# Optimization experiments

Hardware: AMD Instinct MI355X
Metric: run time of the kernel (lower is better)

The kernel has to match this reference:

```python
import jax, jax.numpy as jnp
import numpy as np

N_QUBITS = 14      # must be even (module assert)
IN_CHANNEL = 512   # batch of independent circuits

# PennyLane convention: wire 0 is the most-significant bit of the basis index.

def _mcx_perm(n, c1, c2, t):
    # MultiControlledX with control_values '10': flip target bit t when bit(c1)==1 and bit(c2)==0
    idx = np.arange(2 ** n)
    b1 = (idx >> (n - 1 - c1)) & 1
    b2 = (idx >> (n - 1 - c2)) & 1
    return np.where((b1 == 1) & (b2 == 0), idx ^ (1 << (n - 1 - t)), idx)

_MCX_PERMS = [jnp.asarray(_mcx_perm(N_QUBITS, w, (w + 1) % N_QUBITS, (w + 2) % N_QUBITS))
              for w in range(N_QUBITS)]
# Z-eigenvalue signs per basis state per wire: (2^n, n)
_Z_SIGNS = jnp.asarray(
    np.stack([1.0 - 2.0 * ((np.arange(2 ** N_QUBITS) >> (N_QUBITS - 1 - w)) & 1)
              for w in range(N_QUBITS)], axis=1), dtype=jnp.float32)


def _apply_rx(state, theta, w):
    # RX(theta) = [[cos(t/2), -i sin(t/2)], [-i sin(t/2), cos(t/2)]] on wire w; theta: (B,)
    B = state.shape[0]
    st = state.reshape(B, 2 ** w, 2, -1)
    c = jnp.cos(0.5 * theta)[:, None, None]
    s = (-1j * jnp.sin(0.5 * theta))[:, None, None]
    s0, s1 = st[:, :, 0, :], st[:, :, 1, :]
    out = jnp.stack([c * s0 + s * s1, c * s1 + s * s0], axis=2)
    return out.reshape(B, -1)


def _apply_rz(state, theta, w):
    # RZ(theta) = diag(e^{-i t/2}, e^{+i t/2}) on wire w
    B = state.shape[0]
    st = state.reshape(B, 2 ** w, 2, -1)
    p0 = jnp.exp(-0.5j * theta)[:, None, None]
    p1 = jnp.exp(0.5j * theta)[:, None, None]
    out = jnp.stack([p0 * st[:, :, 0, :], p1 * st[:, :, 1, :]], axis=2)
    return out.reshape(B, -1)


def _apply_isingxx(state, phi, wa, wb):
    a, b = min(wa, wb), max(wa, wb)
    B = state.shape[0]
    st = state.reshape(B, 2 ** a, 2, 2 ** (b - a - 1), 2, -1)
    c = jnp.cos(0.5 * phi)[:, None, None, None]
    s = (-1j * jnp.sin(0.5 * phi))[:, None, None, None]
    s00 = st[:, :, 0, :, 0, :]; s01 = st[:, :, 0, :, 1, :]
    s10 = st[:, :, 1, :, 0, :]; s11 = st[:, :, 1, :, 1, :]
    row0 = jnp.stack([c * s00 + s * s11, c * s01 + s * s10], axis=3)  # (B, 2^a, M, 2, R)
    row1 = jnp.stack([c * s10 + s * s01, c * s11 + s * s00], axis=3)
    return jnp.stack([row0, row1], axis=2).reshape(B, -1)


def _circuit(cp, p):
    n = N_QUBITS
    B = cp.shape[0]
    state = jnp.zeros((B, 2 ** n), dtype=jnp.complex64).at[:, 0].set(1.0)
    for w in range(n):
        state = _apply_rx(state, p[:, 0, w], w)
    for ws in range(n // 2):
        state = _apply_isingxx(state, cp[:, ws], 2 * ws, 2 * ws + 1)
    for w in range(n):
        state = _apply_rz(state, p[:, 1, w], w)
    for ws in range(n // 2):
        wss = 2 * ws + 1
        state = _apply_isingxx(state, cp[:, ws + n // 2], wss, (wss + 1) % n)
    for w in range(n):
        state = _apply_rx(state, p[:, 2, w], w)
    for w in range(n):
        state = state[:, _MCX_PERMS[w]]
    probs = state.real ** 2 + state.imag ** 2  # (B, 2^n)
    return (probs @ _Z_SIGNS).astype(jnp.float32)  # (B, n) = expval PauliZ per wire


def setup_inputs() -> dict:
    key = jax.random.key(0)
    k1, k2 = jax.random.split(key)
    cp = jax.random.uniform(k1, (IN_CHANNEL, N_QUBITS), dtype=jnp.float32) * jnp.pi
    p = jax.random.uniform(k2, (IN_CHANNEL, 3, N_QUBITS), dtype=jnp.float32) * jnp.pi
    return {"cp": cp, "p": p}


def reference(cp, p):
    return _circuit(cp, p)
```

## Files before the change

### kernel.cpp

```cpp
#include <hip/hip_runtime.h>

#define NQ 14
#define NSTATE (1 << NQ)
#define NT 256
#define AMPS 64

typedef float  f2  __attribute__((ext_vector_type(2)));
typedef __fp16 h2v __attribute__((ext_vector_type(2)));

#define N_H2 16640
#define OFF_BTAB  (N_H2*4)
#define OFF_RX3   (OFF_BTAB + 28*8)
#define OFF_XX2   (OFF_RX3 + 28*4)
#define OFF_RED   (OFF_XX2 + 14*4)
#define SMEM_BYTES (OFF_RED + 4*NQ*4)

__device__ __forceinline__ f2 cmul(f2 a, f2 b){
    f2 br = {-b.y, b.x};
    return a.x * b + a.y * br;
}

__device__ __forceinline__ f2 pkswz(f2 ss, f2 y){
    f2 t;
    asm("v_pk_mul_f32 %0, %1, %2 op_sel:[0,1] op_sel_hi:[1,0] neg_hi:[0,1]"
        : "=v"(t) : "v"(ss), "v"(y));
    return t;
}
__device__ __forceinline__ f2 pkfma(f2 a, f2 b, f2 c){
    f2 d;
    asm("v_pk_fma_f32 %0, %1, %2, %3" : "=v"(d) : "v"(a), "v"(b), "v"(c));
    return d;
}
__device__ __forceinline__ void rot2(f2& A, f2& B, f2 cc, f2 ss){
    f2 tA = pkswz(ss, B);
    f2 tB = pkswz(ss, A);
    A = pkfma(cc, A, tA);
    B = pkfma(cc, B, tB);
}

__device__ __forceinline__ h2v pack(f2 v){ return __builtin_amdgcn_cvt_pkrtz(v.x, v.y); }
__device__ __forceinline__ f2  unpack(h2v h){ return (f2){(float)h.x, (float)h.y}; }

template<int CTRL>
__device__ __forceinline__ f2 qperm(f2 v){
    int x = __builtin_amdgcn_mov_dpp(__float_as_int(v.x), CTRL, 0xf, 0xf, true);
    int y = __builtin_amdgcn_mov_dpp(__float_as_int(v.y), CTRL, 0xf, 0xf, true);
    return (f2){__int_as_float(x), __int_as_float(y)};
}

template<int P, int M>
__device__ __forceinline__ void applyXX(f2* amp, f2 cc, f2 ss){
    #pragma unroll
    for (int L = 0; L < AMPS; ++L)
        if (!((L >> P) & 1)) rot2(amp[L], amp[L ^ M], cc, ss);
}
template<int R>
__device__ __forceinline__ void applyRX(f2* amp, f2 cc, f2 ss){
    #pragma unroll
    for (int L = 0; L < AMPS; ++L)
        if (!((L >> R) & 1)) rot2(amp[L], amp[L | (1 << R)], cc, ss);
}

__global__ void perm_tbl_kernel(unsigned short* __restrict__ tbl)
{
    const int j = blockIdx.x * blockDim.x + threadIdx.x;
    int x = j;
    #pragma unroll
    for (int w = 0; w < NQ; ++w) {
        const int p1 = 13 - w;
        const int p2 = 13 - ((w + 1) % NQ);
        const int pt = 13 - ((w + 2) % NQ);
        const int cond = ((x >> p1) & ~(x >> p2)) & 1;
        x ^= cond << pt;
    }
    const int L  = (j >> 1) & 63;
    const int l  = (j & 1) | (((j >> 13) & 1) << 1) | (((j >> 12) & 1) << 2)
                 | (((j >> 11) & 1) << 3) | (((j >> 10) & 1) << 4) | (((j >> 9) & 1) << 5);
    const int w_ = (((j >> 7) & 1) << 1) | ((j >> 8) & 1);
    const int t  = (w_ << 6) | l;
    tbl[(L >> 3) * 2048 + t * 8 + (L & 7)] = (unsigned short)x;
}

__global__ void __launch_bounds__(NT, 2)
qsim_kernel(const float* __restrict__ cp, const float* __restrict__ p,
            const unsigned short* __restrict__ tblD, float* __restrict__ out)
{
    extern __shared__ __align__(16) char smem[];
    h2v* st    = reinterpret_cast<h2v*>(smem);
    f2*  Btab  = reinterpret_cast<f2*>(smem + OFF_BTAB);
    float* rx3c = reinterpret_cast<float*>(smem + OFF_RX3);
    float* rx3s = rx3c + 14;
    float* xx2c = reinterpret_cast<float*>(smem + OFF_XX2);
    float* xx2s = xx2c + 7;
    float* red  = reinterpret_cast<float*>(smem + OFF_RED);

    const int b = blockIdx.x;
    const int t = threadIdx.x;
    const float* pb  = p  + b * 42;
    const float* cpb = cp + b * 14;

    if (t < 7) {
        const int ws = t, wa = 2*ws, wb = 2*ws + 1;
        float sa, ca; sincosf(0.5f * pb[wa], &sa, &ca);
        float sb, cb; sincosf(0.5f * pb[wb], &sb, &cb);
        f2 s00 = {ca*cb, 0.f};
        f2 s01 = {0.f, -ca*sb};
        f2 s10 = {0.f, -sa*cb};
        f2 s11 = {-sa*sb, 0.f};
        float sx, cx; sincosf(0.5f * cpb[ws], &sx, &cx);
        rot2(s00, s11, (f2){cx,cx}, (f2){sx,sx});
        rot2(s01, s10, (f2){cx,cx}, (f2){sx,sx});
        const float ga = 0.5f * pb[14 + wa], gb = 0.5f * pb[14 + wb];
        float sA, cA; sincosf(ga + gb, &sA, &cA);
        float sB, cB; sincosf(gb - ga, &sB, &cB);
        s00 = cmul(s00, (f2){cA, -sA});
        s11 = cmul(s11, (f2){cA,  sA});
        s01 = cmul(s01, (f2){cB,  sB});
        s10 = cmul(s10, (f2){cB, -sB});
        const int k = 6 - ws;
        Btab[k*4+0] = s00; Btab[k*4+1] = s01; Btab[k*4+2] = s10; Btab[k*4+3] = s11;
    } else if (t >= 64 && t < 78) {
        const int w = t - 64;
        float s, c; sincosf(0.5f * pb[28 + w], &s, &c);
        rx3c[w] = c; rx3s[w] = s;
    } else if (t >= 128 && t < 135) {
        const int g = t - 128;
        float s, c; sincosf(0.5f * cpb[7 + g], &s, &c);
        xx2c[g] = c; xx2s[g] = s;
    }
    __syncthreads();

    f2 amp[AMPS];
    f2 cc, ss;
    #define LOADXX(g) do { float c_ = xx2c[g], s_ = xx2s[g]; cc = (f2){c_,c_}; ss = (f2){s_,s_}; } while (0)
    #define LOADRX(w) do { float c_ = rx3c[w], s_ = rx3s[w]; cc = (f2){c_,c_}; ss = (f2){s_,s_}; } while (0)

    {
        const int t6 = (t >> 6) & 1, t7 = t >> 7;
        f2 Pc = cmul(cmul(Btab[t & 3], Btab[4 + ((t >> 2) & 3)]), Btab[8 + ((t >> 4) & 3)]);
        f2 P3a0 = cmul(Pc, Btab[12 + t6]);
        f2 P3a1 = cmul(Pc, Btab[12 + 2 + t6]);
        f2 G00 = cmul(P3a0, Btab[24 + (t7 << 1)]);
        f2 G01 = cmul(P3a0, Btab[24 + (t7 << 1) + 1]);
        f2 G10 = cmul(P3a1, Btab[24 + (t7 << 1)]);
        f2 G11 = cmul(P3a1, Btab[24 + (t7 << 1) + 1]);
        #pragma unroll
        for (int m = 0; m < 16; ++m) {
            f2 H = cmul(Btab[16 + (m & 3)], Btab[20 + (m >> 2)]);
            amp[(m << 1)]          = cmul(G00, H);
            amp[(m << 1) | 1]      = cmul(G10, H);
            amp[32 | (m << 1)]     = cmul(G01, H);
            amp[32 | (m << 1) | 1] = cmul(G11, H);
        }
        LOADXX(0); applyXX<5, 0x30>(amp, cc, ss);
        LOADXX(1); applyXX<3, 0x0C>(amp, cc, ss);
        LOADXX(2); applyXX<1, 0x03>(amp, cc, ss);
        LOADRX(1); applyRX<5>(amp, cc, ss);
        LOADRX(2); applyRX<4>(amp, cc, ss);
        LOADRX(3); applyRX<3>(amp, cc, ss);
        LOADRX(4); applyRX<2>(amp, cc, ss);
        LOADRX(5); applyRX<1>(amp, cc, ss);
        LOADRX(6); applyRX<0>(amp, cc, ss);
        const int jhi = (t7 << 13) | (t & 127);
        #pragma unroll
        for (int L = 0; L < AMPS; ++L) {
            const int j = jhi | (L << 7);
            st[j ^ ((j >> 9) & 31)] = pack(amp[L]);
        }
    }
    __syncthreads();

    {
        uint4 tv[8];
        const uint4* tq = reinterpret_cast<const uint4*>(tblD);
        #pragma unroll
        for (int g = 0; g < 8; ++g) tv[g] = tq[g * 256 + t];

        const int l = t & 63, w_ = t >> 6;
        const int jbase = (l & 1) | (((w_ >> 1) & 1) << 7) | ((w_ & 1) << 8)
                        | (((l >> 5) & 1) << 9) | (((l >> 4) & 1) << 10)
                        | (((l >> 3) & 1) << 11) | (((l >> 2) & 1) << 12)
                        | (((l >> 1) & 1) << 13);
        const int jb2 = jbase ^ ((jbase >> 9) & 31);
        #pragma unroll
        for (int L = 0; L < AMPS; ++L)
            amp[L] = unpack(st[jb2 ^ (L << 1)]);
        LOADXX(3); applyXX<5, 0x30>(amp, cc, ss);
        LOADXX(4); applyXX<3, 0x0C>(amp, cc, ss);
        LOADXX(5); applyXX<1, 0x03>(amp, cc, ss);
        LOADRX(7);  applyRX<5>(amp, cc, ss);
        LOADRX(8);  applyRX<4>(amp, cc, ss);
        LOADRX(9);  applyRX<3>(amp, cc, ss);
        LOADRX(10); applyRX<2>(amp, cc, ss);
        LOADRX(11); applyRX<1>(amp, cc, ss);
        LOADRX(12); applyRX<0>(amp, cc, ss);
        LOADXX(6);
        #pragma unroll
        for (int L = 0; L < AMPS; ++L) { f2 pv = qperm<0x1B>(amp[L]); amp[L] = pkfma(cc, amp[L], pkswz(ss, pv)); }
        LOADRX(13);
        #pragma unroll
        for (int L = 0; L < AMPS; ++L) { f2 pv = qperm<0xB1>(amp[L]); amp[L] = pkfma(cc, amp[L], pkswz(ss, pv)); }
        LOADRX(0);
        #pragma unroll
        for (int L = 0; L < AMPS; ++L) { f2 pv = qperm<0x4E>(amp[L]); amp[L] = pkfma(cc, amp[L], pkswz(ss, pv)); }
        __syncthreads();
        #pragma unroll
        for (int L = 0; L < AMPS; ++L) {
            const unsigned comp = (L & 4) ? ((L & 2) ? tv[L >> 3].w : tv[L >> 3].z)
                                          : ((L & 2) ? tv[L >> 3].y : tv[L >> 3].x);
            const unsigned f = (L & 1) ? (comp >> 16) : (comp & 0xffffu);
            st[f + (f >> 6)] = pack(amp[L]);
        }
    }
    __syncthreads();

    {
        const h2v* erow = st + t * 65;
        float U0, U1 = 0.f, U2 = 0.f, U4, U5, T;
        float C[8];
        float u0acc = 0.f;
        #pragma unroll
        for (int ch = 0; ch < 8; ++ch) {
            float q[8];
            #pragma unroll
            for (int e = 0; e < 8; ++e) {
                const f2 a = unpack(erow[ch * 8 + e]);
                q[e] = fmaf(a.x, a.x, a.y * a.y);
            }
            const float p0 = q[0] + q[1], p1 = q[2] + q[3], p2 = q[4] + q[5], p3 = q[6] + q[7];
            u0acc += (q[1] + q[3]) + (q[5] + q[7]);
            U1 += p1 + p3;
            const float s01 = p0 + p1, s23 = p2 + p3;
            U2 += s23;
            C[ch] = s01 + s23;
        }
        U0 = u0acc;
        {
            const float P0 = C[0] + C[1], P1 = C[2] + C[3], P2 = C[4] + C[5], P3v = C[6] + C[7];
            const float U3v = (C[1] + C[3]) + (C[5] + C[7]);
            U4 = P1 + P3v;
            const float Q0 = P0 + P1, Q1 = P2 + P3v;
            U5 = Q1;
            T = Q0 + Q1;
            C[0] = U3v;
        }
        const float U3 = C[0];

        float s = T;
        float d0, d1, d2, d3, d4, d5;
        {
            float o;
            o = __shfl_xor(s, 1);  d0 = s - o; s += o;
            o = __shfl_xor(d0, 2); d0 += o;
            o = __shfl_xor(s, 2);  d1 = s - o; s += o;
            o = __shfl_xor(d0, 4); d0 += o;
            o = __shfl_xor(d1, 4); d1 += o;
            o = __shfl_xor(s, 4);  d2 = s - o; s += o;
            o = __shfl_xor(d0, 8); d0 += o;
            o = __shfl_xor(d1, 8); d1 += o;
            o = __shfl_xor(d2, 8); d2 += o;
            o = __shfl_xor(s, 8);  d3 = s - o; s += o;
            o = __shfl_xor(d0, 16); d0 += o;
            o = __shfl_xor(d1, 16); d1 += o;
            o = __shfl_xor(d2, 16); d2 += o;
            o = __shfl_xor(d3, 16); d3 += o;
            o = __shfl_xor(s, 16);  d4 = s - o; s += o;
            o = __shfl_xor(d0, 32); d0 += o;
            o = __shfl_xor(d1, 32); d1 += o;
            o = __shfl_xor(d2, 32); d2 += o;
            o = __shfl_xor(d3, 32); d3 += o;
            o = __shfl_xor(d4, 32); d4 += o;
            o = __shfl_xor(s, 32);  d5 = s - o; s += o;
        }
        float V0 = U0, V1 = U1, V2 = U2, V3 = U3, V4 = U4, V5 = U5;
        #pragma unroll
        for (int m = 1; m < 64; m <<= 1) {
            V0 += __shfl_xor(V0, m);
            V1 += __shfl_xor(V1, m);
            V2 += __shfl_xor(V2, m);
            V3 += __shfl_xor(V3, m);
            V4 += __shfl_xor(V4, m);
            V5 += __shfl_xor(V5, m);
        }
        if ((t & 63) == 0) {
            const int wv = t >> 6;
            float* r = red + wv * NQ;
            r[0]  = (wv & 2) ? -s : s;
            r[1]  = (wv & 1) ? -s : s;
            r[2]  = d5;
            r[3]  = d4;
            r[4]  = d3;
            r[5]  = d2;
            r[6]  = d1;
            r[7]  = d0;
            r[8]  = s - 2.f * V5;
            r[9]  = s - 2.f * V4;
            r[10] = s - 2.f * V3;
            r[11] = s - 2.f * V2;
            r[12] = s - 2.f * V1;
            r[13] = s - 2.f * V0;
        }
    }
    __syncthreads();
    if (t < NQ) {
        out[b * NQ + t] = (red[t] + red[NQ + t]) + (red[2 * NQ + t] + red[3 * NQ + t]);
    }
    #undef LOADXX
    #undef LOADRX
}

extern "C" void kernel_launch(void* const* d_in, const int* in_sizes, int n_in,
                              void* d_out, int out_size, void* d_ws, size_t ws_size,
                              hipStream_t stream)
{
    (void)n_in; (void)out_size; (void)ws_size;
    const float* cp = (const float*)d_in[0];
    const float* p  = (const float*)d_in[1];
    float* out = (float*)d_out;
    unsigned short* tbl = (unsigned short*)d_ws;
    const int B = in_sizes[0] / NQ;

    perm_tbl_kernel<<<NSTATE / 256, 256, 0, stream>>>(tbl);

    (void)hipFuncSetAttribute(reinterpret_cast<const void*>(qsim_kernel),
                              hipFuncAttributeMaxDynamicSharedMemorySize, SMEM_BYTES);
    qsim_kernel<<<B, NT, SMEM_BYTES, stream>>>(cp, p, tbl, out);
}
```

Baseline: 80.16 us.

## Rebalance gate split across phases and switch to vectorized swizzled LDS layout

Moves the second XX ring gate and two RX gates into the first register phase by using DPP quad permutes, which rebalances the work between the two LDS transposes. The first store now writes 16-byte packed vectors with an XOR swizzle. The permutation table is re-indexed so each thread loads its own contiguous entries, and the final reduction reads uint4 rows with a padding of 4 per 64 elements. Intra-quad reductions use DPP instead of ds_swizzle shuffles. Shared memory grows slightly, and the remapped index math carries a correctness risk.

Result: faster. 75.44 us (-5.9%).

```diff
diff --git a/kernel.cpp b/kernel.cpp
--- a/kernel.cpp
+++ b/kernel.cpp
@@ -8,7 +8,7 @@
 typedef float  f2  __attribute__((ext_vector_type(2)));
 typedef __fp16 h2v __attribute__((ext_vector_type(2)));
 
-#define N_H2 16640
+#define N_H2 17408
 #define OFF_BTAB  (N_H2*4)
 #define OFF_RX3   (OFF_BTAB + 28*8)
 #define OFF_XX2   (OFF_RX3 + 28*4)
@@ -19,7 +19,6 @@
     f2 br = {-b.y, b.x};
     return a.x * b + a.y * br;
 }
-
 __device__ __forceinline__ f2 pkswz(f2 ss, f2 y){
     f2 t;
     asm("v_pk_mul_f32 %0, %1, %2 op_sel:[0,1] op_sel_hi:[1,0] neg_hi:[0,1]"
@@ -37,15 +36,19 @@
     A = pkfma(cc, A, tA);
     B = pkfma(cc, B, tB);
 }
-
 __device__ __forceinline__ h2v pack(f2 v){ return __builtin_amdgcn_cvt_pkrtz(v.x, v.y); }
 __device__ __forceinline__ f2  unpack(h2v h){ return (f2){(float)h.x, (float)h.y}; }
+__device__ __forceinline__ f2  unpack_u(unsigned w){ h2v h = __builtin_bit_cast(h2v, w); return unpack(h); }
 
 template<int CTRL>
 __device__ __forceinline__ f2 qperm(f2 v){
     int x = __builtin_amdgcn_mov_dpp(__float_as_int(v.x), CTRL, 0xf, 0xf, true);
     int y = __builtin_amdgcn_mov_dpp(__float_as_int(v.y), CTRL, 0xf, 0xf, true);
     return (f2){__int_as_float(x), __int_as_float(y)};
+}
+template<int CTRL>
+__device__ __forceinline__ float fdpp(float v){
+    return __int_as_float(__builtin_amdgcn_mov_dpp(__float_as_int(v), CTRL, 0xf, 0xf, true));
 }
 
 template<int P, int M>
@@ -73,12 +76,9 @@
         const int cond = ((x >> p1) & ~(x >> p2)) & 1;
         x ^= cond << pt;
     }
-    const int L  = (j >> 1) & 63;
-    const int l  = (j & 1) | (((j >> 13) & 1) << 1) | (((j >> 12) & 1) << 2)
-                 | (((j >> 11) & 1) << 3) | (((j >> 10) & 1) << 4) | (((j >> 9) & 1) << 5);
-    const int w_ = (((j >> 7) & 1) << 1) | ((j >> 8) & 1);
-    const int t  = (w_ << 6) | l;
-    tbl[(L >> 3) * 2048 + t * 8 + (L & 7)] = (unsigned short)x;
+    const int t2 = (j >> 5) & 0xFF;
+    const int Lp = ((j >> 13) & 1) | ((j & 31) << 1);
+    tbl[t2 * 64 + Lp] = (unsigned short)x;
 }
 
 __global__ void __launch_bounds__(NT, 2)
@@ -86,8 +86,9 @@
             const unsigned short* __restrict__ tblD, float* __restrict__ out)
 {
     extern __shared__ __align__(16) char smem[];
-    h2v* st    = reinterpret_cast<h2v*>(smem);
-    f2*  Btab  = reinterpret_cast<f2*>(smem + OFF_BTAB);
+    h2v*   st   = reinterpret_cast<h2v*>(smem);
+    uint4* stq  = reinterpret_cast<uint4*>(smem);
+    f2*    Btab = reinterpret_cast<f2*>(smem + OFF_BTAB);
     float* rx3c = reinterpret_cast<float*>(smem + OFF_RX3);
     float* rx3s = rx3c + 14;
     float* xx2c = reinterpret_cast<float*>(smem + OFF_XX2);
@@ -117,8 +118,8 @@
         s11 = cmul(s11, (f2){cA,  sA});
         s01 = cmul(s01, (f2){cB,  sB});
         s10 = cmul(s10, (f2){cB, -sB});
-        const int k = 6 - ws;
-        Btab[k*4+0] = s00; Btab[k*4+1] = s01; Btab[k*4+2] = s10; Btab[k*4+3] = s11;
+        const int g = 6 - ws;
+        Btab[g*4+0] = s00; Btab[g*4+1] = s01; Btab[g*4+2] = s10; Btab[g*4+3] = s11;
     } else if (t >= 64 && t < 78) {
         const int w = t - 64;
         float s, c; sincosf(0.5f * pb[28 + w], &s, &c);
@@ -136,130 +137,128 @@
     #define LOADRX(w) do { float c_ = rx3c[w], s_ = rx3s[w]; cc = (f2){c_,c_}; ss = (f2){s_,s_}; } while (0)
 
     {
-        const int t6 = (t >> 6) & 1, t7 = t >> 7;
-        f2 Pc = cmul(cmul(Btab[t & 3], Btab[4 + ((t >> 2) & 3)]), Btab[8 + ((t >> 4) & 3)]);
-        f2 P3a0 = cmul(Pc, Btab[12 + t6]);
-        f2 P3a1 = cmul(Pc, Btab[12 + 2 + t6]);
-        f2 G00 = cmul(P3a0, Btab[24 + (t7 << 1)]);
-        f2 G01 = cmul(P3a0, Btab[24 + (t7 << 1) + 1]);
-        f2 G10 = cmul(P3a1, Btab[24 + (t7 << 1)]);
-        f2 G11 = cmul(P3a1, Btab[24 + (t7 << 1) + 1]);
+        const int i0 = (((t >> 5) & 1) << 1) | ((t >> 6) & 1);
+        const int i1 = (((t >> 3) & 1) << 1) | ((t >> 4) & 1);
+        const int i2 = (((t >> 1) & 1) << 1) | ((t >> 2) & 1);
+        f2 U = cmul(cmul(Btab[i0], Btab[4 + i1]), Btab[8 + i2]);
+        f2 B3v0 = Btab[12 + (t & 1)];
+        f2 B3v1 = Btab[12 + 2 + (t & 1)];
+        f2 B6v0 = Btab[24 + (((t >> 7) & 1) << 1)];
+        f2 B6v1 = Btab[24 + (((t >> 7) & 1) << 1) + 1];
+        f2 UB0 = cmul(U, B3v0), UB1 = cmul(U, B3v1);
+        f2 W00 = cmul(UB0, B6v0), W01 = cmul(UB1, B6v0);
+        f2 W10 = cmul(UB0, B6v1), W11 = cmul(UB1, B6v1);
         #pragma unroll
         for (int m = 0; m < 16; ++m) {
-            f2 H = cmul(Btab[16 + (m & 3)], Btab[20 + (m >> 2)]);
-            amp[(m << 1)]          = cmul(G00, H);
-            amp[(m << 1) | 1]      = cmul(G10, H);
-            amp[32 | (m << 1)]     = cmul(G01, H);
-            amp[32 | (m << 1) | 1] = cmul(G11, H);
+            f2 H = cmul(Btab[20 + (m >> 2)], Btab[16 + (m & 3)]);
+            amp[(m << 1)]          = cmul(W00, H);
+            amp[(m << 1) | 1]      = cmul(W01, H);
+            amp[32 | (m << 1)]     = cmul(W10, H);
+            amp[32 | (m << 1) | 1] = cmul(W11, H);
         }
         LOADXX(0); applyXX<5, 0x30>(amp, cc, ss);
         LOADXX(1); applyXX<3, 0x0C>(amp, cc, ss);
         LOADXX(2); applyXX<1, 0x03>(amp, cc, ss);
+        LOADXX(3);
+        #pragma unroll
+        for (int L = 0; L < AMPS; ++L) { f2 pv = qperm<0x1B>(amp[L]); amp[L] = pkfma(cc, amp[L], pkswz(ss, pv)); }
         LOADRX(1); applyRX<5>(amp, cc, ss);
         LOADRX(2); applyRX<4>(amp, cc, ss);
         LOADRX(3); applyRX<3>(amp, cc, ss);
         LOADRX(4); applyRX<2>(amp, cc, ss);
         LOADRX(5); applyRX<1>(amp, cc, ss);
         LOADRX(6); applyRX<0>(amp, cc, ss);
-        const int jhi = (t7 << 13) | (t & 127);
-        #pragma unroll
-        for (int L = 0; L < AMPS; ++L) {
-            const int j = jhi | (L << 7);
-            st[j ^ ((j >> 9) & 31)] = pack(amp[L]);
+        LOADRX(7);
+        #pragma unroll
+        for (int L = 0; L < AMPS; ++L) { f2 pv = qperm<0xB1>(amp[L]); amp[L] = pkfma(cc, amp[L], pkswz(ss, pv)); }
+        LOADRX(8);
+        #pragma unroll
+        for (int L = 0; L < AMPS; ++L) { f2 pv = qperm<0x4E>(amp[L]); amp[L] = pkfma(cc, amp[L], pkswz(ss, pv)); }
+        const int w1h = ((t & 1) | ((t >> 1) & 1) << 1 | (((t ^ (t >> 1) ^ (t >> 2)) & 1) << 2));
+        #pragma unroll
+        for (int m = 0; m < 16; ++m) {
+            uint4 pk;
+            pk.x = __builtin_bit_cast(unsigned, pack(amp[4*m]));
+            pk.y = __builtin_bit_cast(unsigned, pack(amp[4*m + 1]));
+            pk.z = __builtin_bit_cast(unsigned, pack(amp[4*m + 2]));
+            pk.w = __builtin_bit_cast(unsigned, pack(amp[4*m + 3]));
+            stq[t * 16 + (m ^ w1h)] = pk;
         }
     }
     __syncthreads();
 
     {
         uint4 tv[8];
-        const uint4* tq = reinterpret_cast<const uint4*>(tblD);
-        #pragma unroll
-        for (int g = 0; g < 8; ++g) tv[g] = tq[g * 256 + t];
-
-        const int l = t & 63, w_ = t >> 6;
-        const int jbase = (l & 1) | (((w_ >> 1) & 1) << 7) | ((w_ & 1) << 8)
-                        | (((l >> 5) & 1) << 9) | (((l >> 4) & 1) << 10)
-                        | (((l >> 3) & 1) << 11) | (((l >> 2) & 1) << 12)
-                        | (((l >> 1) & 1) << 13);
-        const int jb2 = jbase ^ ((jbase >> 9) & 31);
-        #pragma unroll
-        for (int L = 0; L < AMPS; ++L)
-            amp[L] = unpack(st[jb2 ^ (L << 1)]);
-        LOADXX(3); applyXX<5, 0x30>(amp, cc, ss);
-        LOADXX(4); applyXX<3, 0x0C>(amp, cc, ss);
-        LOADXX(5); applyXX<1, 0x03>(amp, cc, ss);
-        LOADRX(7);  applyRX<5>(amp, cc, ss);
-        LOADRX(8);  applyRX<4>(amp, cc, ss);
-        LOADRX(9);  applyRX<3>(amp, cc, ss);
-        LOADRX(10); applyRX<2>(amp, cc, ss);
-        LOADRX(11); applyRX<1>(amp, cc, ss);
-        LOADRX(12); applyRX<0>(amp, cc, ss);
-        LOADXX(6);
-        #pragma unroll
-        for (int L = 0; L < AMPS; ++L) { f2 pv = qperm<0x1B>(amp[L]); amp[L] = pkfma(cc, amp[L], pkswz(ss, pv)); }
-        LOADRX(13);
-        #pragma unroll
-        for (int L = 0; L < AMPS; ++L) { f2 pv = qperm<0xB1>(amp[L]); amp[L] = pkfma(cc, amp[L], pkswz(ss, pv)); }
-        LOADRX(0);
-        #pragma unroll
-        for (int L = 0; L < AMPS; ++L) { f2 pv = qperm<0x4E>(amp[L]); amp[L] = pkfma(cc, amp[L], pkswz(ss, pv)); }
+        {
+            const uint4* tq = reinterpret_cast<const uint4*>(tblD) + t * 8;
+            #pragma unroll
+            for (int g = 0; g < 8; ++g) tv[g] = tq[g];
+        }
+        const int sw2 = ((t & 2) >> 1) | ((t & 1) << 1);
+        const int Lf  = t >> 2;
+        const int w1b = ((sw2 & 1) << 2) | (((sw2 >> 1) & 1) << 3) | ((((sw2 ^ (sw2 >> 1)) & 1)) << 4);
+        #pragma unroll
+        for (int Lp = 0; Lp < AMPS; ++Lp) {
+            const int rev = ((Lp >> 5) & 1) | (((Lp >> 4) & 1) << 1) | (((Lp >> 3) & 1) << 2)
+                          | (((Lp >> 2) & 1) << 3) | (((Lp >> 1) & 1) << 4) | ((Lp & 1) << 5);
+            const int t1  = sw2 | (rev << 2);
+            const int w1v = w1b ^ ((rev & 1) << 4);
+            amp[Lp] = unpack(st[t1 * 64 + (Lf ^ w1v)]);
+        }
+        LOADXX(4); applyXX<5, 0x30>(amp, cc, ss);
+        LOADXX(5); applyXX<3, 0x0C>(amp, cc, ss);
+        LOADXX(6); applyXX<1, 0x03>(amp, cc, ss);
+        LOADRX(9);  applyRX<5>(amp, cc, ss);
+        LOADRX(10); applyRX<4>(amp, cc, ss);
+        LOADRX(11); applyRX<3>(amp, cc, ss);
+        LOADRX(12); applyRX<2>(amp, cc, ss);
+        LOADRX(13); applyRX<1>(amp, cc, ss);
+        LOADRX(0);  applyRX<0>(amp, cc, ss);
         __syncthreads();
         #pragma unroll
-        for (int L = 0; L < AMPS; ++L) {
-            const unsigned comp = (L & 4) ? ((L & 2) ? tv[L >> 3].w : tv[L >> 3].z)
-                                          : ((L & 2) ? tv[L >> 3].y : tv[L >> 3].x);
-            const unsigned f = (L & 1) ? (comp >> 16) : (comp & 0xffffu);
-            st[f + (f >> 6)] = pack(amp[L]);
+        for (int Lp = 0; Lp < AMPS; ++Lp) {
+            const unsigned word = (Lp & 4) ? ((Lp & 2) ? tv[Lp >> 3].w : tv[Lp >> 3].z)
+                                           : ((Lp & 2) ? tv[Lp >> 3].y : tv[Lp >> 3].x);
+            const unsigned f = (Lp & 1) ? (word >> 16) : (word & 0xffffu);
+            st[f + 4 * (f >> 6)] = pack(amp[Lp]);
         }
     }
     __syncthreads();
 
     {
-        const h2v* erow = st + t * 65;
-        float U0, U1 = 0.f, U2 = 0.f, U4, U5, T;
-        float C[8];
-        float u0acc = 0.f;
-        #pragma unroll
-        for (int ch = 0; ch < 8; ++ch) {
-            float q[8];
-            #pragma unroll
-            for (int e = 0; e < 8; ++e) {
-                const f2 a = unpack(erow[ch * 8 + e]);
-                q[e] = fmaf(a.x, a.x, a.y * a.y);
-            }
-            const float p0 = q[0] + q[1], p1 = q[2] + q[3], p2 = q[4] + q[5], p3 = q[6] + q[7];
-            u0acc += (q[1] + q[3]) + (q[5] + q[7]);
-            U1 += p1 + p3;
-            const float s01 = p0 + p1, s23 = p2 + p3;
-            U2 += s23;
-            C[ch] = s01 + s23;
-        }
-        U0 = u0acc;
-        {
-            const float P0 = C[0] + C[1], P1 = C[2] + C[3], P2 = C[4] + C[5], P3v = C[6] + C[7];
-            const float U3v = (C[1] + C[3]) + (C[5] + C[7]);
-            U4 = P1 + P3v;
-            const float Q0 = P0 + P1, Q1 = P2 + P3v;
-            U5 = Q1;
-            T = Q0 + Q1;
-            C[0] = U3v;
-        }
-        const float U3 = C[0];
-
+        float T = 0.f, U0 = 0.f, U1 = 0.f, U2 = 0.f, U3 = 0.f, U4 = 0.f, U5 = 0.f;
+        #pragma unroll
+        for (int m = 0; m < 16; ++m) {
+            const uint4 v = stq[t * 17 + m];
+            const f2 a0 = unpack_u(v.x), a1 = unpack_u(v.y), a2 = unpack_u(v.z), a3 = unpack_u(v.w);
+            const float q0 = fmaf(a0.x, a0.x, a0.y * a0.y);
+            const float q1 = fmaf(a1.x, a1.x, a1.y * a1.y);
+            const float q2 = fmaf(a2.x, a2.x, a2.y * a2.y);
+            const float q3 = fmaf(a3.x, a3.x, a3.y * a3.y);
+            const float t23 = q2 + q3;
+            const float Tc = (q0 + q1) + t23;
+            U0 += q1 + q3;
+            U1 += t23;
+            if (m & 1) U2 += Tc;
+            if (m & 2) U3 += Tc;
+            if (m & 4) U4 += Tc;
+            if (m & 8) U5 += Tc;
+            T += Tc;
+        }
         float s = T;
         float d0, d1, d2, d3, d4, d5;
         {
             float o;
-            o = __shfl_xor(s, 1);  d0 = s - o; s += o;
-            o = __shfl_xor(d0, 2); d0 += o;
-            o = __shfl_xor(s, 2);  d1 = s - o; s += o;
-            o = __shfl_xor(d0, 4); d0 += o;
-            o = __shfl_xor(d1, 4); d1 += o;
-            o = __shfl_xor(s, 4);  d2 = s - o; s += o;
-            o = __shfl_xor(d0, 8); d0 += o;
-            o = __shfl_xor(d1, 8); d1 += o;
-            o = __shfl_xor(d2, 8); d2 += o;
-            o = __shfl_xor(s, 8);  d3 = s - o; s += o;
+            o = fdpp<0xB1>(s);      d0 = s - o; s += o;
+            o = fdpp<0x4E>(d0);     d0 += o;
+            o = fdpp<0x4E>(s);      d1 = s - o; s += o;
+            o = __shfl_xor(d0, 4);  d0 += o;
+            o = __shfl_xor(d1, 4);  d1 += o;
+            o = __shfl_xor(s, 4);   d2 = s - o; s += o;
+            o = __shfl_xor(d0, 8);  d0 += o;
+            o = __shfl_xor(d1, 8);  d1 += o;
+            o = __shfl_xor(d2, 8);  d2 += o;
+            o = __shfl_xor(s, 8);   d3 = s - o; s += o;
             o = __shfl_xor(d0, 16); d0 += o;
             o = __shfl_xor(d1, 16); d1 += o;
             o = __shfl_xor(d2, 16); d2 += o;
@@ -273,8 +272,12 @@
             o = __shfl_xor(s, 32);  d5 = s - o; s += o;
         }
         float V0 = U0, V1 = U1, V2 = U2, V3 = U3, V4 = U4, V5 = U5;
-        #pragma unroll
-        for (int m = 1; m < 64; m <<= 1) {
+        V0 += fdpp<0xB1>(V0); V1 += fdpp<0xB1>(V1); V2 += fdpp<0xB1>(V2);
+        V3 += fdpp<0xB1>(V3); V4 += fdpp<0xB1>(V4); V5 += fdpp<0xB1>(V5);
+        V0 += fdpp<0x4E>(V0); V1 += fdpp<0x4E>(V1); V2 += fdpp<0x4E>(V2);
+        V3 += fdpp<0x4E>(V3); V4 += fdpp<0x4E>(V4); V5 += fdpp<0x4E>(V5);
+        #pragma unroll
+        for (int m = 4; m < 64; m <<= 1) {
             V0 += __shfl_xor(V0, m);
             V1 += __shfl_xor(V1, m);
             V2 += __shfl_xor(V2, m);
```
